# Kernel tuning notes

Hardware: AMD Instinct MI355X
Metric: run time of the kernel (lower is better)

Reference implementation:

```python
import jax, jax.numpy as jnp
import numpy as np

K = 5       # local window size (== scale, so patches are non-overlapping)
SCALE = 5


def setup_inputs() -> dict:
    key = jax.random.key(0)
    k1, k2, k3, k4, k5 = jax.random.split(key, 5)
    B, C, H, W = 4, 64, 128, 128
    feat_q = jax.random.normal(k1, (B, C, H, W), dtype=jnp.float32)
    feat_kv = jax.random.normal(k2, (B, C, H * SCALE, W * SCALE), dtype=jnp.float32)
    s = 0.05
    Wq = jax.random.normal(k3, (C, C), dtype=jnp.float32) * s
    Wk = jax.random.normal(k4, (C, C), dtype=jnp.float32) * s
    Wv = jax.random.normal(k5, (C, C), dtype=jnp.float32) * s
    return {"feat_q": feat_q, "feat_kv": feat_kv, "Wq": Wq, "Wk": Wk, "Wv": Wv}


def _patches(x, B, C, H, W):
    # nn.Unfold(kernel=K, stride=SCALE) with K == SCALE -> non-overlapping KxK
    # blocks, flattened channel-major as (C, kh, kw): [B, C, K*K, H*W]
    x = x.reshape(B, C, H, K, W, K)
    x = x.transpose(0, 1, 3, 5, 2, 4)  # [B, C, K, K, H, W]
    return x.reshape(B, C, K * K, H * W)


def reference(feat_q, feat_kv, Wq, Wk, Wv):
    B, C, H, W = feat_q.shape
    # 1x1 conv projections == channel matmuls
    q = jnp.einsum('oc,bchw->bohw', Wq, feat_q)
    k = jnp.einsum('oc,bchw->bohw', Wk, feat_kv)
    v = jnp.einsum('oc,bchw->bohw', Wv, feat_kv)
    kp = _patches(k, B, C, H, W)   # [B, C, K*K, HW]
    vp = _patches(v, B, C, H, W)   # [B, C, K*K, HW]
    qf = q.reshape(B, C, H * W)    # [B, C, HW]
    # attn[b, l, n] = sum_c q[b,c,l] * k[b,c,n,l]
    attn = jnp.einsum('bcl,bcnl->bln', qf, kp) / jnp.sqrt(jnp.float32(C))
    attn = jax.nn.softmax(attn, axis=-1)
    out = jnp.einsum('bln,bcnl->bcl', attn, vp).reshape(B, C, H, W)
    return feat_q + out
```

## Files before the change

kernel.cpp:

```cpp
#include <hip/hip_runtime.h>
#include <hip/hip_bf16.h>

namespace {

constexpr int C = 64, H = 128, W = 128, HK = 640, WK = 640;
constexpr long long CSTR = (long long)HK * WK;
constexpr int PIX = 8;
constexpr int XD = 5 * PIX;
constexpr int THREADS = 256;

__device__ inline unsigned int packbf2(float lo, float hi) {
    __hip_bfloat162 h2 = __float22bfloat162_rn(make_float2(lo, hi));
    return *reinterpret_cast<unsigned int*>(&h2);
}
__device__ inline float blo(unsigned int u) { return __uint_as_float(u << 16); }
__device__ inline float bhi(unsigned int u) { return __uint_as_float(u & 0xFFFF0000u); }

__global__ void prep_wqk(const float* __restrict__ Wq, const float* __restrict__ Wk,
                         float* __restrict__ Wqk) {
    int tid = blockIdx.x * 256 + threadIdx.x;
    int i = tid >> 6, j = tid & 63;
    float acc = 0.f;
    #pragma unroll 8
    for (int c = 0; c < 64; ++c) acc = fmaf(Wk[c * 64 + i], Wq[c * 64 + j], acc);
    Wqk[i * 64 + j] = 0.125f * acc;
}

__global__ __launch_bounds__(THREADS, 5)
void cag_fused(const float* __restrict__ fq, const float* __restrict__ fkv,
               const float* __restrict__ Wqk, const float* __restrict__ Wv,
               float* __restrict__ out) {
    __shared__ unsigned int slab[5 * XD * 32];
    __shared__ float fq_lds[PIX * 68];
    __shared__ float qk_lds[PIX * 68];
    __shared__ float lg[PIX * 26];
    __shared__ unsigned int wsum[PIX * 36];

    const int t = threadIdx.x;
    const int bid = blockIdx.x;
    const int wb = bid & 15;
    const int h  = (bid >> 4) & 127;
    const int b  = bid >> 11;
    const int row0 = 5 * h, col0 = XD * wb, w0q = PIX * wb;

    {
        const int p = t & 7, c = t >> 3;
        fq_lds[p * 68 + c]      = fq[((size_t)(b * 64 + c) << 14) + h * 128 + w0q + p];
        fq_lds[p * 68 + c + 32] = fq[((size_t)(b * 64 + c + 32) << 14) + h * 128 + w0q + p];
    }
    {
        const float* kvb = fkv + (size_t)b * C * CSTR;
        for (int i = t; i < 800; i += THREADS) {
            const int x4 = i % 10;
            const int y  = (i / 10) % 5;
            const int c4 = i / 50;
            const int xb = 4 * x4;
            const float* g = kvb + (size_t)(4 * c4) * CSTR
                           + (size_t)(row0 + y) * WK + (col0 + xb);
            float4 F0 = *(const float4*)(g);
            float4 F1 = *(const float4*)(g + CSTR);
            float4 F2 = *(const float4*)(g + 2 * CSTR);
            float4 F3 = *(const float4*)(g + 3 * CSTR);
            const float* f0 = (const float*)&F0; const float* f1 = (const float*)&F1;
            const float* f2 = (const float*)&F2; const float* f3 = (const float*)&F3;
            #pragma unroll
            for (int dx = 0; dx < 4; ++dx) {
                const int x = xb + dx;
                const int base = (y * XD + x) * 32;
                const int sw = (((x & 7) ^ y) << 2);
                slab[base + ((2 * c4)     ^ sw)] = packbf2(f0[dx], f1[dx]);
                slab[base + ((2 * c4 + 1) ^ sw)] = packbf2(f2[dx], f3[dx]);
            }
        }
    }
    __syncthreads();

    {
        const int l = t & 7, i0 = t >> 3;
        const float4* wr0 = (const float4*)(Wqk + i0 * 64);
        const float4* wr1 = (const float4*)(Wqk + (i0 + 32) * 64);
        const float4* fv  = (const float4*)(fq_lds + l * 68);
        float a0 = 0.f, a1 = 0.f;
        #pragma unroll
        for (int j = 0; j < 16; ++j) {
            float4 f = fv[j], w0 = wr0[j], w1 = wr1[j];
            a0 = fmaf(w0.x, f.x, a0); a0 = fmaf(w0.y, f.y, a0);
            a0 = fmaf(w0.z, f.z, a0); a0 = fmaf(w0.w, f.w, a0);
            a1 = fmaf(w1.x, f.x, a1); a1 = fmaf(w1.y, f.y, a1);
            a1 = fmaf(w1.z, f.z, a1); a1 = fmaf(w1.w, f.w, a1);
        }
        qk_lds[l * 68 + i0]      = a0;
        qk_lds[l * 68 + i0 + 32] = a1;
    }
    __syncthreads();

    {
        const int l = t >> 5;
        const int n = t & 31;
        float v = -1e30f;
        if (n < 25) {
            const int ky = n / 5, kx = n - 5 * (n / 5);
            const int x = 5 * l + kx;
            const int base = (ky * XD + x) * 32;
            const int sw7 = (x & 7) ^ ky;
            const float4* qv = (const float4*)(qk_lds + l * 68);
            float acc = 0.f;
            #pragma unroll
            for (int j = 0; j < 8; ++j) {
                uint4 u = *(const uint4*)&slab[base + 4 * (j ^ sw7)];
                float4 qa = qv[2 * j], qb = qv[2 * j + 1];
                acc = fmaf(qa.x, blo(u.x), acc); acc = fmaf(qa.y, bhi(u.x), acc);
                acc = fmaf(qa.z, blo(u.y), acc); acc = fmaf(qa.w, bhi(u.y), acc);
                acc = fmaf(qb.x, blo(u.z), acc); acc = fmaf(qb.y, bhi(u.z), acc);
                acc = fmaf(qb.z, blo(u.w), acc); acc = fmaf(qb.w, bhi(u.w), acc);
            }
            v = acc;
        }
        float m = v;
        #pragma unroll
        for (int off = 16; off; off >>= 1) m = fmaxf(m, __shfl_xor(m, off, 32));
        float e = __expf(v - m);
        float s = e;
        #pragma unroll
        for (int off = 16; off; off >>= 1) s += __shfl_xor(s, off, 32);
        if (n < 25) lg[l * 26 + n] = e / s;
    }
    __syncthreads();

    {
        const int l = t >> 5, s = t & 31;
        float alo = 0.f, ahi = 0.f;
        #pragma unroll
        for (int n2 = 0; n2 < 25; ++n2) {
            const int ky = n2 / 5, kx = n2 - 5 * ky;
            const int x = 5 * l + kx;
            const unsigned int u = slab[(ky * XD + x) * 32 + (s ^ ((((x & 7) ^ ky)) << 2))];
            const float a = lg[l * 26 + n2];
            alo = fmaf(a, blo(u), alo);
            ahi = fmaf(a, bhi(u), ahi);
        }
        wsum[l * 36 + s] = packbf2(alo, ahi);
    }
    __syncthreads();

    {
        const int p = t & 7, o0 = t >> 3;
        const uint4* wsr = (const uint4*)(wsum + p * 36);
        float vals[64];
        #pragma unroll
        for (int g8 = 0; g8 < 8; ++g8) {
            uint4 u = wsr[g8];
            vals[8 * g8 + 0] = blo(u.x); vals[8 * g8 + 1] = bhi(u.x);
            vals[8 * g8 + 2] = blo(u.y); vals[8 * g8 + 3] = bhi(u.y);
            vals[8 * g8 + 4] = blo(u.z); vals[8 * g8 + 5] = bhi(u.z);
            vals[8 * g8 + 6] = blo(u.w); vals[8 * g8 + 7] = bhi(u.w);
        }
        const float4* wv0 = (const float4*)(Wv + o0 * 64);
        const float4* wv1 = (const float4*)(Wv + (o0 + 32) * 64);
        float a0 = fq_lds[p * 68 + o0];
        float a1 = fq_lds[p * 68 + o0 + 32];
        #pragma unroll
        for (int j = 0; j < 16; ++j) {
            float4 w0 = wv0[j], w1 = wv1[j];
            a0 = fmaf(w0.x, vals[4 * j + 0], a0); a0 = fmaf(w0.y, vals[4 * j + 1], a0);
            a0 = fmaf(w0.z, vals[4 * j + 2], a0); a0 = fmaf(w0.w, vals[4 * j + 3], a0);
            a1 = fmaf(w1.x, vals[4 * j + 0], a1); a1 = fmaf(w1.y, vals[4 * j + 1], a1);
            a1 = fmaf(w1.z, vals[4 * j + 2], a1); a1 = fmaf(w1.w, vals[4 * j + 3], a1);
        }
        const size_t ob = ((size_t)(b * 64 + o0) << 14) + h * 128 + w0q + p;
        out[ob] = a0;
        out[ob + ((size_t)32 << 14)] = a1;
    }
}

}

extern "C" void kernel_launch(void* const* d_in, const int* in_sizes, int n_in,
                              void* d_out, int out_size, void* d_ws, size_t ws_size,
                              hipStream_t stream) {
    (void)in_sizes; (void)n_in; (void)ws_size; (void)out_size;
    const float* fq  = (const float*)d_in[0];
    const float* fkv = (const float*)d_in[1];
    const float* Wq  = (const float*)d_in[2];
    const float* Wk  = (const float*)d_in[3];
    const float* Wv  = (const float*)d_in[4];
    float* out = (float*)d_out;
    float* Wqk = (float*)d_ws;

    prep_wqk <<<dim3(16),    dim3(256),     0, stream>>>(Wq, Wk, Wqk);
    cag_fused<<<dim3(8192),  dim3(THREADS), 0, stream>>>(fq, fkv, Wqk, Wv, out);
}
```

Before: 157.1 us.

## Make fused kernel persistent with double-buffered async global-to-LDS tile loads

Replaces the 8192 one-shot blocks with 256 persistent 512-thread blocks, each looping over 32 tiles. The next tile's fp32 data is prefetched straight into LDS with global_load_lds while the current tile is converted to swizzled bf16 and processed, so memory latency overlaps compute. The per-tile work is re-split across 8 wavefronts, one per pixel, using cross-half shuffles. The cost is one block per CU, a large dynamic LDS footprint, an extra LDS conversion pass and fewer resident waves to hide latency.

```diff
diff --git a/kernel.cpp b/kernel.cpp
--- a/kernel.cpp
+++ b/kernel.cpp
@@ -1,13 +1,26 @@
 #include <hip/hip_runtime.h>
 #include <hip/hip_bf16.h>
+#include <stdint.h>
 
 namespace {
 
 constexpr int C = 64, H = 128, W = 128, HK = 640, WK = 640;
 constexpr long long CSTR = (long long)HK * WK;
 constexpr int PIX = 8;
-constexpr int XD = 5 * PIX;
-constexpr int THREADS = 256;
+constexpr int NT = 32;
+constexpr int THREADS = 512;
+
+constexpr int OF_SLABF = 0;
+constexpr int OF_SLABB = 25600;
+constexpr int OF_FQ    = OF_SLABB + 6400;
+constexpr int OF_QKW   = OF_FQ + 1088;
+constexpr int OF_LG    = OF_QKW + 512;
+constexpr int OF_WSW   = OF_LG + 208;
+constexpr int SMEM_U32 = OF_WSW + 512;
+constexpr int SMEM_BYTES = SMEM_U32 * 4;
+
+typedef __attribute__((address_space(1))) const void glob_void;
+typedef __attribute__((address_space(3))) void lds_void;
 
 __device__ inline unsigned int packbf2(float lo, float hi) {
     __hip_bfloat162 h2 = __float22bfloat162_rn(make_float2(lo, hi));
@@ -15,6 +28,17 @@
 }
 __device__ inline float blo(unsigned int u) { return __uint_as_float(u << 16); }
 __device__ inline float bhi(unsigned int u) { return __uint_as_float(u & 0xFFFF0000u); }
+
+__device__ inline void barrier_lds() {
+    asm volatile("s_waitcnt lgkmcnt(0)" ::: "memory");
+    __builtin_amdgcn_s_barrier();
+    __builtin_amdgcn_sched_barrier(0);
+}
+__device__ inline void barrier_all() {
+    asm volatile("s_waitcnt vmcnt(0) lgkmcnt(0)" ::: "memory");
+    __builtin_amdgcn_s_barrier();
+    __builtin_amdgcn_sched_barrier(0);
+}
 
 __global__ void prep_wqk(const float* __restrict__ Wq, const float* __restrict__ Wk,
                          float* __restrict__ Wqk) {
@@ -26,150 +50,165 @@
     Wqk[i * 64 + j] = 0.125f * acc;
 }
 
-__global__ __launch_bounds__(THREADS, 5)
+__global__ __launch_bounds__(THREADS, 1)
 void cag_fused(const float* __restrict__ fq, const float* __restrict__ fkv,
                const float* __restrict__ Wqk, const float* __restrict__ Wv,
                float* __restrict__ out) {
-    __shared__ unsigned int slab[5 * XD * 32];
-    __shared__ float fq_lds[PIX * 68];
-    __shared__ float qk_lds[PIX * 68];
-    __shared__ float lg[PIX * 26];
-    __shared__ unsigned int wsum[PIX * 36];
-
-    const int t = threadIdx.x;
-    const int bid = blockIdx.x;
-    const int wb = bid & 15;
-    const int h  = (bid >> 4) & 127;
-    const int b  = bid >> 11;
-    const int row0 = 5 * h, col0 = XD * wb, w0q = PIX * wb;
-
+    extern __shared__ uint32_t sm[];
+    uint32_t* slabf = sm + OF_SLABF;
+    uint32_t* slabb = sm + OF_SLABB;
+    float*    fqld  = (float*)(sm + OF_FQ);
+    float*    qkw   = (float*)(sm + OF_QKW);
+    float*    lg    = (float*)(sm + OF_LG);
+    float*    wsw   = (float*)(sm + OF_WSW);
+
+    const int t    = threadIdx.x;
+    const int wv   = t >> 6;
+    const int lane = t & 63;
+    const int bid  = blockIdx.x;
+
+    auto issue_tile = [&](int tt, int d) {
+        int r = (tt < 16) ? bid : bid + 256;
+        int b = r >> 7, h = r & 127;
+        const float* kvb = fkv + (size_t)b * C * CSTR + (size_t)(5 * h) * WK
+                         + 40 * (tt & 15);
+        uint32_t* dst = slabf + d * 12800;
+        for (int q = wv; q < 50; q += 8) {
+            int L   = q * 256 + lane * 4;
+            int rr  = L / 40;
+            int col = L - rr * 40;
+            int c   = rr / 5;
+            int y   = rr - c * 5;
+            const float* gp = kvb + (size_t)c * CSTR + (size_t)y * WK + col;
+            __builtin_amdgcn_global_load_lds((glob_void*)gp, (lds_void*)(dst + q * 256),
+                                             16, 0, 0);
+        }
+    };
+
+    issue_tile(0, 0);
     {
-        const int p = t & 7, c = t >> 3;
-        fq_lds[p * 68 + c]      = fq[((size_t)(b * 64 + c) << 14) + h * 128 + w0q + p];
-        fq_lds[p * 68 + c + 32] = fq[((size_t)(b * 64 + c + 32) << 14) + h * 128 + w0q + p];
+        int b0 = bid >> 7, h0 = bid & 127;
+        float v = fq[((size_t)(b0 * 64 + (t >> 3)) << 14) + h0 * 128 + (t & 7)];
+        fqld[(t & 7) * 68 + (t >> 3)] = v;
     }
-    {
-        const float* kvb = fkv + (size_t)b * C * CSTR;
-        for (int i = t; i < 800; i += THREADS) {
-            const int x4 = i % 10;
-            const int y  = (i / 10) % 5;
-            const int c4 = i / 50;
-            const int xb = 4 * x4;
-            const float* g = kvb + (size_t)(4 * c4) * CSTR
-                           + (size_t)(row0 + y) * WK + (col0 + xb);
-            float4 F0 = *(const float4*)(g);
-            float4 F1 = *(const float4*)(g + CSTR);
-            float4 F2 = *(const float4*)(g + 2 * CSTR);
-            float4 F3 = *(const float4*)(g + 3 * CSTR);
-            const float* f0 = (const float*)&F0; const float* f1 = (const float*)&F1;
-            const float* f2 = (const float*)&F2; const float* f3 = (const float*)&F3;
-            #pragma unroll
-            for (int dx = 0; dx < 4; ++dx) {
-                const int x = xb + dx;
-                const int base = (y * XD + x) * 32;
-                const int sw = (((x & 7) ^ y) << 2);
-                slab[base + ((2 * c4)     ^ sw)] = packbf2(f0[dx], f1[dx]);
-                slab[base + ((2 * c4 + 1) ^ sw)] = packbf2(f2[dx], f3[dx]);
-            }
-        }
-    }
-    __syncthreads();
-
-    {
-        const int l = t & 7, i0 = t >> 3;
-        const float4* wr0 = (const float4*)(Wqk + i0 * 64);
-        const float4* wr1 = (const float4*)(Wqk + (i0 + 32) * 64);
-        const float4* fv  = (const float4*)(fq_lds + l * 68);
-        float a0 = 0.f, a1 = 0.f;
-        #pragma unroll
-        for (int j = 0; j < 16; ++j) {
-            float4 f = fv[j], w0 = wr0[j], w1 = wr1[j];
-            a0 = fmaf(w0.x, f.x, a0); a0 = fmaf(w0.y, f.y, a0);
-            a0 = fmaf(w0.z, f.z, a0); a0 = fmaf(w0.w, f.w, a0);
-            a1 = fmaf(w1.x, f.x, a1); a1 = fmaf(w1.y, f.y, a1);
-            a1 = fmaf(w1.z, f.z, a1); a1 = fmaf(w1.w, f.w, a1);
-        }
-        qk_lds[l * 68 + i0]      = a0;
-        qk_lds[l * 68 + i0 + 32] = a1;
-    }
-    __syncthreads();
-
-    {
-        const int l = t >> 5;
-        const int n = t & 31;
-        float v = -1e30f;
-        if (n < 25) {
-            const int ky = n / 5, kx = n - 5 * (n / 5);
-            const int x = 5 * l + kx;
-            const int base = (ky * XD + x) * 32;
-            const int sw7 = (x & 7) ^ ky;
-            const float4* qv = (const float4*)(qk_lds + l * 68);
+    barrier_all();
+
+    for (int tile = 0; tile < NT; ++tile) {
+        const int cur = tile & 1, nxt = cur ^ 1;
+        const int r   = (tile < 16) ? bid : bid + 256;
+        const int b   = r >> 7, h = r & 127;
+        const int w0q = 8 * (tile & 15);
+
+        float fq2 = 0.f;
+        if (tile + 1 < NT) {
+            issue_tile(tile + 1, nxt);
+            int r2 = (tile + 1 < 16) ? bid : bid + 256;
+            int b2 = r2 >> 7, h2 = r2 & 127;
+            fq2 = fq[((size_t)(b2 * 64 + (t >> 3)) << 14) + h2 * 128
+                     + 8 * ((tile + 1) & 15) + (t & 7)];
+        }
+
+        {
+            const float* sf = (const float*)(slabf + cur * 12800);
+            for (int i = t; i < 6400; i += THREADS) {
+                int x  = i % 40;
+                int y  = (i / 40) % 5;
+                int cp = i / 200;
+                float f0 = sf[(2 * cp) * 200 + y * 40 + x];
+                float f1 = sf[(2 * cp + 1) * 200 + y * 40 + x];
+                slabb[(y * 40 + x) * 32 + (cp ^ ((((x & 7) ^ y)) << 2))] = packbf2(f0, f1);
+            }
+        }
+        barrier_lds();
+
+        {
+            const float4* wr = (const float4*)(Wqk + lane * 64);
+            const float4* fv = (const float4*)(fqld + cur * 544 + wv * 68);
+            float qv = 0.f;
+            #pragma unroll
+            for (int j = 0; j < 16; ++j) {
+                float4 f = fv[j], wq = wr[j];
+                qv = fmaf(wq.x, f.x, qv); qv = fmaf(wq.y, f.y, qv);
+                qv = fmaf(wq.z, f.z, qv); qv = fmaf(wq.w, f.w, qv);
+            }
+            qkw[wv * 64 + lane] = qv;
+        }
+
+        {
+            const int n = lane & 31, ch = lane >> 5;
             float acc = 0.f;
-            #pragma unroll
-            for (int j = 0; j < 8; ++j) {
-                uint4 u = *(const uint4*)&slab[base + 4 * (j ^ sw7)];
-                float4 qa = qv[2 * j], qb = qv[2 * j + 1];
-                acc = fmaf(qa.x, blo(u.x), acc); acc = fmaf(qa.y, bhi(u.x), acc);
-                acc = fmaf(qa.z, blo(u.y), acc); acc = fmaf(qa.w, bhi(u.y), acc);
-                acc = fmaf(qb.x, blo(u.z), acc); acc = fmaf(qb.y, bhi(u.z), acc);
-                acc = fmaf(qb.z, blo(u.w), acc); acc = fmaf(qb.w, bhi(u.w), acc);
-            }
-            v = acc;
-        }
-        float m = v;
-        #pragma unroll
-        for (int off = 16; off; off >>= 1) m = fmaxf(m, __shfl_xor(m, off, 32));
-        float e = __expf(v - m);
-        float s = e;
-        #pragma unroll
-        for (int off = 16; off; off >>= 1) s += __shfl_xor(s, off, 32);
-        if (n < 25) lg[l * 26 + n] = e / s;
-    }
-    __syncthreads();
-
-    {
-        const int l = t >> 5, s = t & 31;
-        float alo = 0.f, ahi = 0.f;
-        #pragma unroll
-        for (int n2 = 0; n2 < 25; ++n2) {
-            const int ky = n2 / 5, kx = n2 - 5 * ky;
-            const int x = 5 * l + kx;
-            const unsigned int u = slab[(ky * XD + x) * 32 + (s ^ ((((x & 7) ^ ky)) << 2))];
-            const float a = lg[l * 26 + n2];
-            alo = fmaf(a, blo(u), alo);
-            ahi = fmaf(a, bhi(u), ahi);
-        }
-        wsum[l * 36 + s] = packbf2(alo, ahi);
-    }
-    __syncthreads();
-
-    {
-        const int p = t & 7, o0 = t >> 3;
-        const uint4* wsr = (const uint4*)(wsum + p * 36);
-        float vals[64];
-        #pragma unroll
-        for (int g8 = 0; g8 < 8; ++g8) {
-            uint4 u = wsr[g8];
-            vals[8 * g8 + 0] = blo(u.x); vals[8 * g8 + 1] = bhi(u.x);
-            vals[8 * g8 + 2] = blo(u.y); vals[8 * g8 + 3] = bhi(u.y);
-            vals[8 * g8 + 4] = blo(u.z); vals[8 * g8 + 5] = bhi(u.z);
-            vals[8 * g8 + 6] = blo(u.w); vals[8 * g8 + 7] = bhi(u.w);
-        }
-        const float4* wv0 = (const float4*)(Wv + o0 * 64);
-        const float4* wv1 = (const float4*)(Wv + (o0 + 32) * 64);
-        float a0 = fq_lds[p * 68 + o0];
-        float a1 = fq_lds[p * 68 + o0 + 32];
-        #pragma unroll
-        for (int j = 0; j < 16; ++j) {
-            float4 w0 = wv0[j], w1 = wv1[j];
-            a0 = fmaf(w0.x, vals[4 * j + 0], a0); a0 = fmaf(w0.y, vals[4 * j + 1], a0);
-            a0 = fmaf(w0.z, vals[4 * j + 2], a0); a0 = fmaf(w0.w, vals[4 * j + 3], a0);
-            a1 = fmaf(w1.x, vals[4 * j + 0], a1); a1 = fmaf(w1.y, vals[4 * j + 1], a1);
-            a1 = fmaf(w1.z, vals[4 * j + 2], a1); a1 = fmaf(w1.w, vals[4 * j + 3], a1);
-        }
-        const size_t ob = ((size_t)(b * 64 + o0) << 14) + h * 128 + w0q + p;
-        out[ob] = a0;
-        out[ob + ((size_t)32 << 14)] = a1;
+            if (n < 25) {
+                const int ky = n / 5, kx = n - 5 * (n / 5);
+                const int x = 5 * wv + kx;
+                const int base = (ky * 40 + x) * 32;
+                const int sw7 = (x & 7) ^ ky;
+                const float4* qg = (const float4*)(qkw + wv * 64);
+                #pragma unroll
+                for (int jj = 0; jj < 4; ++jj) {
+                    const int j = ch * 4 + jj;
+                    uint4 u = *(const uint4*)&slabb[base + 4 * (j ^ sw7)];
+                    float4 qa = qg[2 * j], qb = qg[2 * j + 1];
+                    acc = fmaf(qa.x, blo(u.x), acc); acc = fmaf(qa.y, bhi(u.x), acc);
+                    acc = fmaf(qa.z, blo(u.y), acc); acc = fmaf(qa.w, bhi(u.y), acc);
+                    acc = fmaf(qb.x, blo(u.z), acc); acc = fmaf(qb.y, bhi(u.z), acc);
+                    acc = fmaf(qb.z, blo(u.w), acc); acc = fmaf(qb.w, bhi(u.w), acc);
+                }
+            }
+            acc += __shfl_xor(acc, 32, 64);
+            float v = (n < 25) ? acc : -1e30f;
+            float m = v;
+            #pragma unroll
+            for (int off = 16; off; off >>= 1) m = fmaxf(m, __shfl_xor(m, off, 32));
+            float e = __expf(v - m);
+            float ssum = e;
+            #pragma unroll
+            for (int off = 16; off; off >>= 1) ssum += __shfl_xor(ssum, off, 32);
+            if (ch == 0 && n < 25) lg[wv * 26 + n] = e / ssum;
+        }
+
+        {
+            const int s = lane & 31, nh = lane >> 5;
+            float alo = 0.f, ahi = 0.f;
+            #define WS_STEP(n)                                                        \
+                { constexpr int ky = (n) / 5, kx = (n) % 5;                           \
+                  const int x = 5 * wv + kx;                                          \
+                  unsigned int u = slabb[(ky * 40 + x) * 32                           \
+                                         + (s ^ ((((x & 7) ^ ky)) << 2))];            \
+                  float a = lg[wv * 26 + (n)];                                        \
+                  alo = fmaf(a, blo(u), alo); ahi = fmaf(a, bhi(u), ahi); }
+            if (nh == 0) {
+                WS_STEP(0) WS_STEP(1) WS_STEP(2) WS_STEP(3) WS_STEP(4) WS_STEP(5)
+                WS_STEP(6) WS_STEP(7) WS_STEP(8) WS_STEP(9) WS_STEP(10) WS_STEP(11)
+                WS_STEP(12)
+            } else {
+                WS_STEP(13) WS_STEP(14) WS_STEP(15) WS_STEP(16) WS_STEP(17)
+                WS_STEP(18) WS_STEP(19) WS_STEP(20) WS_STEP(21) WS_STEP(22)
+                WS_STEP(23) WS_STEP(24)
+            }
+            #undef WS_STEP
+            alo += __shfl_xor(alo, 32, 64);
+            ahi += __shfl_xor(ahi, 32, 64);
+            if (nh == 0) {
+                wsw[wv * 64 + 2 * s]     = alo;
+                wsw[wv * 64 + 2 * s + 1] = ahi;
+            }
+        }
+
+        {
+            const float4* wvr = (const float4*)(Wv + lane * 64);
+            const float4* wsr = (const float4*)(wsw + wv * 64);
+            float a0 = fqld[cur * 544 + wv * 68 + lane];
+            #pragma unroll
+            for (int j = 0; j < 16; ++j) {
+                float4 s4 = wsr[j], w4 = wvr[j];
+                a0 = fmaf(w4.x, s4.x, a0); a0 = fmaf(w4.y, s4.y, a0);
+                a0 = fmaf(w4.z, s4.z, a0); a0 = fmaf(w4.w, s4.w, a0);
+            }
+            out[((size_t)(b * 64 + lane) << 14) + h * 128 + w0q + wv] = a0;
+        }
+
+        if (tile + 1 < NT) fqld[nxt * 544 + (t & 7) * 68 + (t >> 3)] = fq2;
+        barrier_all();
     }
 }
 
@@ -187,6 +226,11 @@
     float* out = (float*)d_out;
     float* Wqk = (float*)d_ws;
 
-    prep_wqk <<<dim3(16),    dim3(256),     0, stream>>>(Wq, Wk, Wqk);
-    cag_fused<<<dim3(8192),  dim3(THREADS), 0, stream>>>(fq, fkv, Wqk, Wv, out);
-}
+    static_assert(SMEM_BYTES <= 160 * 1024, "LDS overflow");
+    hipError_t err_ = hipFuncSetAttribute(reinterpret_cast<const void*>(&cag_fused),
+                        hipFuncAttributeMaxDynamicSharedMemorySize, SMEM_BYTES);
+    (void)err_;
+
+    prep_wqk <<<dim3(16),  dim3(256),     0,          stream>>>(Wq, Wk, Wqk);
+    cag_fused<<<dim3(256), dim3(THREADS), SMEM_BYTES, stream>>>(fq, fkv, Wqk, Wv, out);
+}
```

Result: slower. 368.4 us (+134.4%).
